# Performance work log

Hardware: AMD Instinct MI355X
Metric: run time of the kernel (lower is better)

The kernel has to match this reference:

```python
import jax, jax.numpy as jnp
import numpy as np
from jax import lax

N_ITER = 64
RESIDUAL_SCALE = 0.1


def setup_inputs() -> dict:
    key = jax.random.key(0)
    ks = jax.random.split(key, 5)
    # seed initialized as randn * 0.1 per the module; conv weights scaled small so
    # 64 residual iterations remain numerically stable (mimics trained-net scale).
    seed = jax.random.normal(ks[0], (1, 1, 8, 8), jnp.float32) * 0.1
    w1 = jax.random.normal(ks[1], (16, 1, 3, 3), jnp.float32) * (1.0 / 3.0)  # ~kaiming, fan_in=9
    b1 = jax.random.normal(ks[2], (16,), jnp.float32) * 0.1
    w2 = jax.random.normal(ks[3], (1, 16, 1, 1), jnp.float32) * 0.25  # fan_in=16
    b2 = jax.random.normal(ks[4], (1,), jnp.float32) * 0.1
    return {"seed": seed, "w1": w1, "b1": b1, "w2": w2, "b2": b2,
            "rows": 768, "cols": 768}


def _rules(x, w1, b1, w2, b2):
    # Conv2d(1,16,3,pad=1) -> GELU(exact erf, torch default) -> Conv2d(16,1,1)
    h = lax.conv_general_dilated(x, w1, (1, 1), 'SAME',
                                 dimension_numbers=('NCHW', 'OIHW', 'NCHW'))
    h = jax.nn.gelu(h + b1[None, :, None, None], approximate=False)
    y = lax.conv_general_dilated(h, w2, (1, 1), 'SAME',
                                 dimension_numbers=('NCHW', 'OIHW', 'NCHW'))
    return y + b2[None, :, None, None]


def reference(seed, w1, b1, w2, b2, rows, cols):
    # F.interpolate(mode='bilinear', align_corners=False) == jax.image.resize
    # 'bilinear' (both use half-pixel centers).
    x = jax.image.resize(seed, (1, 1, rows, cols), method='bilinear')

    def step(x, _):
        return x + _rules(x, w1, b1, w2, b2) * RESIDUAL_SCALE, None

    x, _ = lax.scan(step, x, None, length=N_ITER)
    return x[0, 0]  # (rows, cols)
```

## Files before the change

kernel.cpp:

```cpp
#include <hip/hip_runtime.h>
#include <math.h>

#define IMG 768
#define TX 48
#define TY 24
#define KF 4
#define ITX (TX + 2 * KF)
#define ITY (TY + 2 * KF)
#define NBX (IMG / TX)
#define NBY (IMG / TY)
#define NT 448
#define RES_SCALE 0.1f
#define NITER 64

#define TAB_N 256
#define TAB_D (5.8f / 256.0f)
#define TAB_SCALE (256.0f / 5.8f)

__device__ __forceinline__ float erf_hp(float t) {
    float e = __builtin_amdgcn_exp2f(t * t * -0.72134752044448f);
    float kk = __builtin_amdgcn_rcpf(fmaf(0.23164188662f, t, 1.0f));
    float p = fmaf(1.061405429f, kk, -1.453152027f);
    p = fmaf(p, kk, 1.421413741f);
    p = fmaf(p, kk, -0.284496736f);
    p = fmaf(p, kk, 0.254829592f);
    p *= kk;
    return fmaf(-e, p, 1.0f);
}

__device__ __forceinline__ float gelu2_lut(float x, const float2* __restrict__ tab) {
    float aa = fminf(fabsf(x) * TAB_SCALE, 255.999f);
    float2 ts = tab[(int)aa];
    float r = fmaf(aa, ts.y, ts.x);
    return fmaf(fabsf(x), r, x);
}

__device__ __forceinline__ float bilinear8(const float* __restrict__ seed,
                                           int gy, int gx) {
    float sy = fmaf((float)gy, 0.0104166667f, -0.4947916667f);
    float sx = fmaf((float)gx, 0.0104166667f, -0.4947916667f);
    float fy = floorf(sy), fx = floorf(sx);
    float wy = sy - fy, wx = sx - fx;
    int y0 = (int)fy, x0 = (int)fx;
    int y0c = min(max(y0, 0), 7), y1c = min(max(y0 + 1, 0), 7);
    int x0c = min(max(x0, 0), 7), x1c = min(max(x0 + 1, 0), 7);
    float v00 = seed[y0c * 8 + x0c], v01 = seed[y0c * 8 + x1c];
    float v10 = seed[y1c * 8 + x0c], v11 = seed[y1c * 8 + x1c];
    float top = v00 + wx * (v01 - v00);
    float bot = v10 + wx * (v11 - v10);
    return top + wy * (bot - top);
}

template <bool FIRST>
__global__ void __launch_bounds__(NT)
__attribute__((amdgpu_waves_per_eu(2, 4)))
fused_steps(
        const float* __restrict__ seed,
        const float* __restrict__ xin, float* __restrict__ xout,
        const float* __restrict__ gw1, const float* __restrict__ gb1,
        const float* __restrict__ gw2, const float* __restrict__ gb2) {
    __shared__ float buf[2][ITY * ITX];
    __shared__ float2 gtab[TAB_N];
    const int tid = threadIdx.x;
    const int bx = blockIdx.x % NBX, by = blockIdx.x / NBX;
    const int gx0 = bx * TX - KF, gy0 = by * TY - KF;
    const bool border = (bx == 0) | (bx == NBX - 1) | (by == 0) | (by == NBY - 1);

    if (tid < TAB_N) {
        float t0 = tid * TAB_D;
        float e0 = erf_hp(t0);
        float de = erf_hp(t0 + TAB_D) - e0;
        gtab[tid] = make_float2(fmaf(-de, (float)tid, e0), de);
    }

    if (FIRST) {
        for (int t = tid; t < ITY * ITX; t += NT) {
            int r = t / ITX, c = t - r * ITX;
            int gy = gy0 + r, gx = gx0 + c;
            float v = 0.0f;
            if (gy >= 0 && gy < IMG && gx >= 0 && gx < IMG)
                v = bilinear8(seed, gy, gx);
            buf[0][t] = v;
        }
    } else if (!border) {
        int r = tid / (ITX / 4), c4 = tid - r * (ITX / 4);
        *reinterpret_cast<float4*>(&buf[0][r * ITX + c4 * 4]) =
            *reinterpret_cast<const float4*>(&xin[(gy0 + r) * IMG + gx0 + c4 * 4]);
    } else {
        for (int t = tid; t < ITY * ITX; t += NT) {
            int r = t / ITX, c = t - r * ITX;
            int gy = gy0 + r, gx = gx0 + c;
            float v = 0.0f;
            if (gy >= 0 && gy < IMG && gx >= 0 && gx < IMG) v = xin[gy * IMG + gx];
            buf[0][t] = v;
        }
    }
    __syncthreads();

    const float b2v = gb2[0];

    float vb[16], w2h[16];
#pragma unroll
    for (int ch = 0; ch < 16; ++ch) { vb[ch] = gb1[ch]; w2h[ch] = gw2[ch] * 0.5f; }
    asm volatile("" : "+v"(vb[0]), "+v"(vb[1]), "+v"(vb[2]), "+v"(vb[3]),
                      "+v"(vb[4]), "+v"(vb[5]), "+v"(vb[6]), "+v"(vb[7]),
                      "+v"(vb[8]), "+v"(vb[9]), "+v"(vb[10]), "+v"(vb[11]),
                      "+v"(vb[12]), "+v"(vb[13]), "+v"(vb[14]), "+v"(vb[15]));
    asm volatile("" : "+v"(w2h[0]), "+v"(w2h[1]), "+v"(w2h[2]), "+v"(w2h[3]),
                      "+v"(w2h[4]), "+v"(w2h[5]), "+v"(w2h[6]), "+v"(w2h[7]),
                      "+v"(w2h[8]), "+v"(w2h[9]), "+v"(w2h[10]), "+v"(w2h[11]),
                      "+v"(w2h[12]), "+v"(w2h[13]), "+v"(w2h[14]), "+v"(w2h[15]));

#pragma unroll
    for (int j = 0; j < KF; ++j) {
        const int SX = ITX - 2 - 2 * j;
        const int SY = ITY - 2 - 2 * j;
        const int off = j + 1;
        const int total = SX * SY;
        const int B = (total + NT - 1) / NT;
        const float* __restrict__ src = &buf[j & 1][0];
        float* __restrict__ dst = &buf[(j & 1) ^ 1][0];

#pragma unroll
        for (int k = 0; k < B; ++k) {
            int p = tid + k * NT;
            bool ok = p < total;
            if (!ok) p = total - 1;
            int q = p / SX;
            int r = off + q, c = off + (p - q * SX);
            const float* s0 = &src[(r - 1) * ITX + (c - 1)];
            float n0 = s0[0],           n1 = s0[1],           n2 = s0[2];
            float n3 = s0[ITX],         n4 = s0[ITX + 1],     n5 = s0[ITX + 2];
            float n6 = s0[2 * ITX],     n7 = s0[2 * ITX + 1], n8 = s0[2 * ITX + 2];

            float h[16];
#pragma unroll
            for (int ch = 0; ch < 16; ++ch) {
                const float* wc = &gw1[ch * 9];
                float t = fmaf(wc[0], n0, vb[ch]);
                t = fmaf(wc[1], n1, t);
                t = fmaf(wc[2], n2, t);
                t = fmaf(wc[3], n3, t);
                t = fmaf(wc[4], n4, t);
                t = fmaf(wc[5], n5, t);
                t = fmaf(wc[6], n6, t);
                t = fmaf(wc[7], n7, t);
                t = fmaf(wc[8], n8, t);
                h[ch] = t;
            }
            asm volatile("" : "+v"(h[0]), "+v"(h[1]), "+v"(h[2]), "+v"(h[3]),
                              "+v"(h[4]), "+v"(h[5]), "+v"(h[6]), "+v"(h[7]),
                              "+v"(h[8]), "+v"(h[9]), "+v"(h[10]), "+v"(h[11]),
                              "+v"(h[12]), "+v"(h[13]), "+v"(h[14]), "+v"(h[15]));

            float y = b2v;
#pragma unroll
            for (int ch = 0; ch < 16; ++ch)
                y = fmaf(w2h[ch], gelu2_lut(h[ch], gtab), y);

            float v = fmaf(RES_SCALE, y, n4);
            if (border) {
                int gy = gy0 + r, gx = gx0 + c;
                bool inimg = (gy >= 0) & (gy < IMG) & (gx >= 0) & (gx < IMG);
                if (!inimg) v = 0.0f;
            }
            if (ok) dst[r * ITX + c] = v;
        }
        __syncthreads();
    }

    {
        int t = tid;
        if (t < (TX / 4) * TY) {
            int r = t / (TX / 4), c4 = t - r * (TX / 4);
            *reinterpret_cast<float4*>(&xout[(gy0 + KF + r) * IMG + gx0 + KF + c4 * 4]) =
                *reinterpret_cast<const float4*>(&buf[0][(KF + r) * ITX + KF + c4 * 4]);
        }
    }
}

extern "C" void kernel_launch(void* const* d_in, const int* in_sizes, int n_in,
                              void* d_out, int out_size, void* d_ws, size_t ws_size,
                              hipStream_t stream) {
    const float* seed = (const float*)d_in[0];
    const float* w1   = (const float*)d_in[1];
    const float* b1   = (const float*)d_in[2];
    const float* w2   = (const float*)d_in[3];
    const float* b2   = (const float*)d_in[4];

    float* out = (float*)d_out;
    float* ws  = (float*)d_ws;

    float* a = out;
    float* b = ws;
    fused_steps<true><<<NBX * NBY, NT, 0, stream>>>(seed, a, b, w1, b1, w2, b2);
    { float* t = a; a = b; b = t; }
    for (int it = KF; it < NITER; it += KF) {
        fused_steps<false><<<NBX * NBY, NT, 0, stream>>>(seed, a, b, w1, b1, w2, b2);
        float* t = a; a = b; b = t;
    }
}
```

Before: 410.9 us.

## Use packed FP32 FMAs for 3x3 conv and interleave pixels per channel

Rewrites the per-pixel conv1 loop so that each channel's 9 taps are computed with packed two-wide float FMAs, using pre-paired neighbour vectors and aligned weight pairs (even/odd channel layouts). It also restructures the loop to hold all pixels of a thread (up to 4) at once and iterate channels outermost, so weight loads are shared across pixels and GELU/accumulate work can interleave. The GELU scale factor is folded into the final residual constant. The added per-pixel vector registers raise register pressure, and summation order changes slightly.

```diff
diff --git a/kernel.cpp b/kernel.cpp
--- a/kernel.cpp
+++ b/kernel.cpp
@@ -12,6 +12,8 @@
 #define NT 448
 #define RES_SCALE 0.1f
 #define NITER 64
+
+typedef float v2f __attribute__((ext_vector_type(2)));
 
 #define TAB_N 256
 #define TAB_D (5.8f / 256.0f)
@@ -97,19 +99,15 @@
     }
     __syncthreads();
 
-    const float b2v = gb2[0];
-
-    float vb[16], w2h[16];
-#pragma unroll
-    for (int ch = 0; ch < 16; ++ch) { vb[ch] = gb1[ch]; w2h[ch] = gw2[ch] * 0.5f; }
+    const float y0init = 2.0f * gb2[0];
+
+    float vb[16];
+#pragma unroll
+    for (int ch = 0; ch < 16; ++ch) vb[ch] = gb1[ch];
     asm volatile("" : "+v"(vb[0]), "+v"(vb[1]), "+v"(vb[2]), "+v"(vb[3]),
                       "+v"(vb[4]), "+v"(vb[5]), "+v"(vb[6]), "+v"(vb[7]),
                       "+v"(vb[8]), "+v"(vb[9]), "+v"(vb[10]), "+v"(vb[11]),
                       "+v"(vb[12]), "+v"(vb[13]), "+v"(vb[14]), "+v"(vb[15]));
-    asm volatile("" : "+v"(w2h[0]), "+v"(w2h[1]), "+v"(w2h[2]), "+v"(w2h[3]),
-                      "+v"(w2h[4]), "+v"(w2h[5]), "+v"(w2h[6]), "+v"(w2h[7]),
-                      "+v"(w2h[8]), "+v"(w2h[9]), "+v"(w2h[10]), "+v"(w2h[11]),
-                      "+v"(w2h[12]), "+v"(w2h[13]), "+v"(w2h[14]), "+v"(w2h[15]));
 
 #pragma unroll
     for (int j = 0; j < KF; ++j) {
@@ -121,50 +119,97 @@
         const float* __restrict__ src = &buf[j & 1][0];
         float* __restrict__ dst = &buf[(j & 1) ^ 1][0];
 
+        int rr[4], cc[4];
+        bool ok[4];
+        v2f e0_[4], e1_[4], e2_[4], e3_[4], o0_[4], o1_[4], o2_[4], o3_[4];
+        float n0s[4], n8s[4];
 #pragma unroll
         for (int k = 0; k < B; ++k) {
             int p = tid + k * NT;
-            bool ok = p < total;
-            if (!ok) p = total - 1;
+            ok[k] = p < total;
+            if (!ok[k]) p = total - 1;
             int q = p / SX;
-            int r = off + q, c = off + (p - q * SX);
-            const float* s0 = &src[(r - 1) * ITX + (c - 1)];
-            float n0 = s0[0],           n1 = s0[1],           n2 = s0[2];
-            float n3 = s0[ITX],         n4 = s0[ITX + 1],     n5 = s0[ITX + 2];
-            float n6 = s0[2 * ITX],     n7 = s0[2 * ITX + 1], n8 = s0[2 * ITX + 2];
-
-            float h[16];
-#pragma unroll
-            for (int ch = 0; ch < 16; ++ch) {
+            rr[k] = off + q;
+            cc[k] = off + (p - q * SX);
+            const float* s0 = &src[(rr[k] - 1) * ITX + (cc[k] - 1)];
+            v2f t;
+            t.x = s0[0];   t.y = s0[1];   e0_[k] = t;
+            t.x = s0[2];   t.y = s0[56];  e1_[k] = t;
+            t.x = s0[57];  t.y = s0[58];  e2_[k] = t;
+            t.x = s0[112]; t.y = s0[113]; e3_[k] = t;
+            t.x = s0[1];   t.y = s0[2];   o0_[k] = t;
+            t.x = s0[56];  t.y = s0[57];  o1_[k] = t;
+            t.x = s0[58];  t.y = s0[112]; o2_[k] = t;
+            t.x = s0[113]; t.y = s0[114]; o3_[k] = t;
+            n0s[k] = s0[0];
+            n8s[k] = s0[114];
+        }
+        float y[4];
+#pragma unroll
+        for (int k = 0; k < B; ++k) y[k] = y0init;
+
+#pragma unroll
+        for (int cp = 0; cp < 8; ++cp) {
+            {
+                const int ch = 2 * cp;
                 const float* wc = &gw1[ch * 9];
-                float t = fmaf(wc[0], n0, vb[ch]);
-                t = fmaf(wc[1], n1, t);
-                t = fmaf(wc[2], n2, t);
-                t = fmaf(wc[3], n3, t);
-                t = fmaf(wc[4], n4, t);
-                t = fmaf(wc[5], n5, t);
-                t = fmaf(wc[6], n6, t);
-                t = fmaf(wc[7], n7, t);
-                t = fmaf(wc[8], n8, t);
-                h[ch] = t;
+                v2f w01 = *reinterpret_cast<const v2f*>(wc + 0);
+                v2f w23 = *reinterpret_cast<const v2f*>(wc + 2);
+                v2f w45 = *reinterpret_cast<const v2f*>(wc + 4);
+                v2f w67 = *reinterpret_cast<const v2f*>(wc + 6);
+                const float w8 = wc[8];
+                const float w2c = gw2[ch];
+                float h[4];
+#pragma unroll
+                for (int k = 0; k < B; ++k) {
+                    v2f a = w01 * e0_[k];
+                    a = __builtin_elementwise_fma(w23, e1_[k], a);
+                    a = __builtin_elementwise_fma(w45, e2_[k], a);
+                    a = __builtin_elementwise_fma(w67, e3_[k], a);
+                    h[k] = fmaf(w8, n8s[k], vb[ch]) + a.x + a.y;
+                }
+                if (B == 4) asm volatile("" : "+v"(h[0]), "+v"(h[1]), "+v"(h[2]), "+v"(h[3]));
+                else        asm volatile("" : "+v"(h[0]), "+v"(h[1]), "+v"(h[2]));
+#pragma unroll
+                for (int k = 0; k < B; ++k)
+                    y[k] = fmaf(w2c, gelu2_lut(h[k], gtab), y[k]);
             }
-            asm volatile("" : "+v"(h[0]), "+v"(h[1]), "+v"(h[2]), "+v"(h[3]),
-                              "+v"(h[4]), "+v"(h[5]), "+v"(h[6]), "+v"(h[7]),
-                              "+v"(h[8]), "+v"(h[9]), "+v"(h[10]), "+v"(h[11]),
-                              "+v"(h[12]), "+v"(h[13]), "+v"(h[14]), "+v"(h[15]));
-
-            float y = b2v;
-#pragma unroll
-            for (int ch = 0; ch < 16; ++ch)
-                y = fmaf(w2h[ch], gelu2_lut(h[ch], gtab), y);
-
-            float v = fmaf(RES_SCALE, y, n4);
+            {
+                const int ch = 2 * cp + 1;
+                const float* wc = &gw1[ch * 9];
+                const float w0 = wc[0];
+                v2f w12 = *reinterpret_cast<const v2f*>(wc + 1);
+                v2f w34 = *reinterpret_cast<const v2f*>(wc + 3);
+                v2f w56 = *reinterpret_cast<const v2f*>(wc + 5);
+                v2f w78 = *reinterpret_cast<const v2f*>(wc + 7);
+                const float w2c = gw2[ch];
+                float h[4];
+#pragma unroll
+                for (int k = 0; k < B; ++k) {
+                    v2f a = w12 * o0_[k];
+                    a = __builtin_elementwise_fma(w34, o1_[k], a);
+                    a = __builtin_elementwise_fma(w56, o2_[k], a);
+                    a = __builtin_elementwise_fma(w78, o3_[k], a);
+                    h[k] = fmaf(w0, n0s[k], vb[ch]) + a.x + a.y;
+                }
+                if (B == 4) asm volatile("" : "+v"(h[0]), "+v"(h[1]), "+v"(h[2]), "+v"(h[3]));
+                else        asm volatile("" : "+v"(h[0]), "+v"(h[1]), "+v"(h[2]));
+#pragma unroll
+                for (int k = 0; k < B; ++k)
+                    y[k] = fmaf(w2c, gelu2_lut(h[k], gtab), y[k]);
+            }
+        }
+
+#pragma unroll
+        for (int k = 0; k < B; ++k) {
+            float n4 = e2_[k].x;
+            float v = fmaf(0.05f, y[k], n4);
             if (border) {
-                int gy = gy0 + r, gx = gx0 + c;
+                int gy = gy0 + rr[k], gx = gx0 + cc[k];
                 bool inimg = (gy >= 0) & (gy < IMG) & (gx >= 0) & (gx < IMG);
                 if (!inimg) v = 0.0f;
             }
-            if (ok) dst[r * ITX + c] = v;
+            if (ok[k]) dst[rr[k] * ITX + cc[k]] = v;
         }
         __syncthreads();
     }
```

After: 608.3 us. 48.0% more time.
